# Optimization experiments

Measured on AMD Instinct MI355X. Metric: run time of the kernel, lower is better.

## Reference

```python
import jax, jax.numpy as jnp
import numpy as np

N_ATOMS = 50000
N_EDGES = 1_600_000
N_MOL = 500
HIDDEN = 128
FILTERS = 128
GAUSS = 50
LAYERS = 3
CUTOFF = 10.0
LOG2 = 0.6931471805599453


def ssp(x):
    # ShiftedSoftplus: softplus(x) - log(2)
    return jax.nn.softplus(x) - LOG2


def setup_inputs() -> dict:
    key = jax.random.key(0)
    ks = jax.random.split(key, 24)
    z = jax.random.randint(ks[0], (N_ATOMS,), 0, 100)
    pos = jax.random.uniform(ks[1], (N_ATOMS, 3), jnp.float32) * 5.0  # box keeps d < cutoff
    batch = jnp.sort(jax.random.randint(ks[2], (N_ATOMS,), 0, N_MOL))
    row = jax.random.randint(ks[3], (N_EDGES,), 0, N_ATOMS)
    off = jax.random.randint(ks[4], (N_EDGES,), 1, N_ATOMS)
    col = (row + off) % N_ATOMS  # guarantees row != col (no zero distances)
    edge_index = jnp.stack([row, col])
    def lin(k, fi, fo):
        return jax.random.normal(k, (fi, fo), jnp.float32) * (1.0 / np.sqrt(fi))
    emb = jax.random.normal(ks[5], (100, HIDDEN), jnp.float32)
    mlp1_w = jnp.stack([lin(jax.random.fold_in(ks[6], i), GAUSS, FILTERS) for i in range(LAYERS)])
    mlp1_b = jnp.zeros((LAYERS, FILTERS), jnp.float32)
    mlp2_w = jnp.stack([lin(jax.random.fold_in(ks[7], i), FILTERS, FILTERS) for i in range(LAYERS)])
    mlp2_b = jnp.zeros((LAYERS, FILTERS), jnp.float32)
    lin1_w = jnp.stack([lin(jax.random.fold_in(ks[8], i), HIDDEN, FILTERS) for i in range(LAYERS)])
    lin2_w = jnp.stack([lin(jax.random.fold_in(ks[9], i), FILTERS, HIDDEN) for i in range(LAYERS)])
    lin2_b = jnp.zeros((LAYERS, HIDDEN), jnp.float32)
    int_w = jnp.stack([lin(jax.random.fold_in(ks[10], i), HIDDEN, HIDDEN) for i in range(LAYERS)])
    int_b = jnp.zeros((LAYERS, HIDDEN), jnp.float32)
    out1_w = lin(ks[11], HIDDEN, HIDDEN // 2)
    out1_b = jnp.zeros((HIDDEN // 2,), jnp.float32)
    out2_w = lin(ks[12], HIDDEN // 2, 1)
    out2_b = jnp.zeros((1,), jnp.float32)
    return {"z": z, "pos": pos, "batch": batch, "edge_index": edge_index,
            "emb": emb, "mlp1_w": mlp1_w, "mlp1_b": mlp1_b, "mlp2_w": mlp2_w, "mlp2_b": mlp2_b,
            "lin1_w": lin1_w, "lin2_w": lin2_w, "lin2_b": lin2_b, "int_w": int_w, "int_b": int_b,
            "out1_w": out1_w, "out1_b": out1_b, "out2_w": out2_w, "out2_b": out2_b}


def reference(z, pos, batch, edge_index, emb, mlp1_w, mlp1_b, mlp2_w, mlp2_b,
              lin1_w, lin2_w, lin2_b, int_w, int_b, out1_w, out1_b, out2_w, out2_b):
    row, col = edge_index[0], edge_index[1]  # source j, target i
    d = jnp.linalg.norm(pos[row] - pos[col], axis=-1)  # [E]
    # GaussianSmearing
    offset = jnp.linspace(0.0, CUTOFF, GAUSS)
    coeff = -0.5 / (offset[1] - offset[0]) ** 2
    rbf = jnp.exp(coeff * (d[:, None] - offset[None, :]) ** 2)  # [E, GAUSS]
    # cosine cutoff
    C = 0.5 * (jnp.cos(d * jnp.pi / CUTOFF) + 1.0)  # [E]
    h = emb[z]  # [N, H]
    for l in range(LAYERS):
        W = ssp(rbf @ mlp1_w[l] + mlp1_b[l]) @ mlp2_w[l] + mlp2_b[l]  # [E, F]
        W = W * C[:, None]
        x = h @ lin1_w[l]                 # [N, F]
        msg = x[row] * W                  # gather from source, per-edge filter
        agg = jax.ops.segment_sum(msg, col, num_segments=N_ATOMS)  # scatter-add to targets
        x = agg @ lin2_w[l] + lin2_b[l]
        x = ssp(x)
        x = x @ int_w[l] + int_b[l]
        h = h + x                         # residual
    h = ssp(h @ out1_w + out1_b)
    h = h @ out2_w + out2_b               # [N, 1] per-atom energy
    out = jax.ops.segment_sum(h[:, 0], batch, num_segments=N_MOL)  # 'add' readout
    return out.reshape(-1)
```

## Files before the change

kernel.cpp:

```cpp
#include <hip/hip_runtime.h>
#include <math.h>

#define HID 128
#define NGAUSS 50
#define TBL 2048
#define TBL2 8192
#define DMAX 8.6605f
#define LDX 136
#define PGRID 768

typedef _Float16 h4 __attribute__((ext_vector_type(4)));
typedef _Float16 f16x8 __attribute__((ext_vector_type(8)));
typedef float f32x4 __attribute__((ext_vector_type(4)));

__device__ __forceinline__ float sspf(float x) {
  float ax = fabsf(x);
  return fmaxf(x, 0.0f) + log1pf(expf(-ax)) - 0.69314718055994530942f;
}

__global__ __launch_bounds__(128) void build_table_k(
    const float* __restrict__ w1, const float* __restrict__ b1,
    const float* __restrict__ w2, const float* __restrict__ b2,
    float* __restrict__ tab) {
  int l = blockIdx.x >> 11;
  int ti = blockIdx.x & (TBL - 1);
  int j = threadIdx.x;
  __shared__ float rbf[NGAUSS];
  __shared__ float v1[HID];
  const float step = DMAX / (float)(TBL - 1);
  float d = ti * step;
  if (j < NGAUSS) {
    const float gstep = 10.0f / 49.0f;
    const float gcoeff = -12.005f;
    float diff = d - j * gstep;
    rbf[j] = expf(gcoeff * diff * diff);
  }
  __syncthreads();
  float s = b1[l * HID + j];
  const float* w1p = w1 + l * NGAUSS * HID + j;
  for (int g = 0; g < NGAUSS; g++) s = fmaf(rbf[g], w1p[g * HID], s);
  v1[j] = sspf(s);
  __syncthreads();
  float s2 = b2[l * HID + j];
  const float* w2p = w2 + l * HID * HID + j;
  for (int k = 0; k < HID; k++) s2 = fmaf(v1[k], w2p[k * HID], s2);
  float C = 0.5f * (cosf(d * 0.3141592653589793f) + 1.0f);
  tab[((size_t)l * TBL + ti) * HID + j] = s2 * C;
}

__global__ __launch_bounds__(256) void upsample_k(
    const float* __restrict__ tab, _Float16* __restrict__ tabh) {
  int idx = blockIdx.x * 256 + threadIdx.x;
  if (idx >= 3 * TBL2 * HID) return;
  int ch = idx & 127;
  int i = (idx >> 7) & (TBL2 - 1);
  int l = idx >> 20;
  float t = (float)i * ((float)(TBL - 1) / (float)(TBL2 - 1));
  int i0 = min((int)t, TBL - 2);
  float f = t - (float)i0;
  const float* base = tab + ((size_t)l * TBL + i0) * HID + ch;
  tabh[idx] = (_Float16)fmaf(f, base[HID] - base[0], base[0]);
}

__global__ __launch_bounds__(256) void wswz10_k(
    const float* __restrict__ lin1, const float* __restrict__ lin2,
    const float* __restrict__ intw, const float* __restrict__ out1w,
    _Float16* __restrict__ out) {
  int b = blockIdx.x;
  int t = threadIdx.x;
  if (b < 9) {
    const float* src = (b < 3 ? lin1 : (b < 6 ? lin2 : intw)) + (size_t)(b % 3) * HID * HID;
    _Float16* dst = out + (size_t)b * 16384;
    for (int i = t; i < 16384; i += 256) {
      int j = i & 7;
      int lane = (i >> 3) & 63;
      int kk = (i >> 9) & 3;
      int ntc = i >> 11;
      int n = ntc * 16 + (lane & 15);
      int k = kk * 32 + (lane >> 4) * 8 + j;
      dst[i] = (_Float16)src[k * HID + n];
    }
  } else {
    _Float16* dst = out + (size_t)9 * 16384;
    for (int i = t; i < 8192; i += 256) {
      int j = i & 7;
      int lane = (i >> 3) & 63;
      int kk = (i >> 9) & 3;
      int ntc = i >> 11;
      int n = ntc * 16 + (lane & 15);
      int k = kk * 32 + (lane >> 4) * 8 + j;
      dst[i] = (_Float16)out1w[k * 64 + n];
    }
  }
}

__global__ __launch_bounds__(256) void emb_gather_k(
    const int* __restrict__ z, const float* __restrict__ emb,
    float* __restrict__ h, int N) {
  int i4 = blockIdx.x * 256 + threadIdx.x;
  if (i4 >= N * 32) return;
  int a = i4 >> 5;
  ((float4*)h)[i4] = ((const float4*)emb)[z[a] * 32 + (i4 & 31)];
}

__global__ __launch_bounds__(256) void bcount_k(
    const int* __restrict__ col, int* __restrict__ bcount, int E, int nbuck) {
  __shared__ int hist[1024];
  int t = threadIdx.x;
  int e0 = blockIdx.x * 2048;
  for (int j = t; j < nbuck; j += 256) hist[j] = 0;
  __syncthreads();
#pragma unroll
  for (int u = 0; u < 8; u++) {
    int e = e0 + u * 256 + t;
    if (e < E) atomicAdd(&hist[col[e] >> 6], 1);
  }
  __syncthreads();
  for (int j = t; j < nbuck; j += 256)
    if (hist[j]) atomicAdd(&bcount[j], hist[j]);
}

__global__ __launch_bounds__(256) void bucket_scan_k(
    const int* __restrict__ bcount, int* __restrict__ bstart,
    int* __restrict__ bcur, int nbuck, int* __restrict__ starts, int N) {
  __shared__ int sh[256];
  int t = threadIdx.x;
  int chunk = (nbuck + 255) / 256;
  int b0 = t * chunk;
  int c[8];
  int s = 0;
  for (int j = 0; j < chunk; j++) {
    int idx = b0 + j;
    int v = (idx < nbuck) ? bcount[idx] : 0;
    c[j] = v;
    s += v;
  }
  sh[t] = s;
  __syncthreads();
  for (int o = 1; o < 256; o <<= 1) {
    int v = (t >= o) ? sh[t - o] : 0;
    __syncthreads();
    sh[t] += v;
    __syncthreads();
  }
  int p = (t == 0) ? 0 : sh[t - 1];
  for (int j = 0; j < chunk; j++) {
    int idx = b0 + j;
    if (idx < nbuck) {
      bstart[idx] = p;
      bcur[idx] = p;
      p += c[j];
    }
  }
  if (t == 255) {
    bstart[nbuck] = p;
    starts[N] = p;
  }
}

__global__ __launch_bounds__(256) void scatterA_k(
    const int* __restrict__ row, const int* __restrict__ col,
    const float* __restrict__ pos, int* __restrict__ bcur,
    unsigned long long* __restrict__ tmp, int E, int nbuck) {
  __shared__ int hist[1024];
  __shared__ int base[1024];
  int t = threadIdx.x;
  int e0 = blockIdx.x * 2048;
  for (int j = t; j < nbuck; j += 256) hist[j] = 0;
  __syncthreads();
  int bkt[8];
  int rnk[8];
  unsigned long long key[8];
#pragma unroll
  for (int u = 0; u < 8; u++) {
    int e = e0 + u * 256 + t;
    bkt[u] = -1;
    if (e < E) {
      int r = row[e], c = col[e];
      float dx = pos[r * 3 + 0] - pos[c * 3 + 0];
      float dy = pos[r * 3 + 1] - pos[c * 3 + 1];
      float dz = pos[r * 3 + 2] - pos[c * 3 + 2];
      float d = sqrtf(dx * dx + dy * dy + dz * dz);
      const float inv2 = (float)(TBL2 - 1) / DMAX;
      int q = min((int)(d * inv2 + 0.5f), TBL2 - 1);
      unsigned int pay = ((unsigned int)r << 13) | (unsigned int)q;
      key[u] = ((unsigned long long)pay << 6) | (unsigned long long)(c & 63);
      bkt[u] = c >> 6;
      rnk[u] = atomicAdd(&hist[bkt[u]], 1);
    }
  }
  __syncthreads();
  for (int j = t; j < nbuck; j += 256)
    base[j] = hist[j] ? atomicAdd(&bcur[j], hist[j]) : 0;
  __syncthreads();
#pragma unroll
  for (int u = 0; u < 8; u++)
    if (bkt[u] >= 0) tmp[(size_t)base[bkt[u]] + rnk[u]] = key[u];
}

__global__ __launch_bounds__(256) void scatterB_k(
    const unsigned long long* __restrict__ tmp, const int* __restrict__ bstart,
    int* __restrict__ starts, unsigned int* __restrict__ payload, int N) {
  int j = blockIdx.x;
  int t = threadIdx.x;
  __shared__ int cnt[64];
  __shared__ int cur[64];
  int rs = bstart[j], re = bstart[j + 1];
  if (t < 64) cnt[t] = 0;
  __syncthreads();
  for (int e = rs + t; e < re; e += 256)
    atomicAdd(&cnt[(int)(tmp[e] & 63)], 1);
  __syncthreads();
  if (t < 64) {
    int mine = cnt[t];
    int v = mine;
    for (int o = 1; o < 64; o <<= 1) {
      int u = __shfl_up(v, o, 64);
      if (t >= o) v += u;
    }
    int excl = v - mine;
    int c = j * 64 + t;
    if (c < N) starts[c] = rs + excl;
    cur[t] = rs + excl;
  }
  __syncthreads();
  for (int e = rs + t; e < re; e += 256) {
    unsigned long long k = tmp[e];
    int p = atomicAdd(&cur[(int)(k & 63)], 1);
    payload[p] = (unsigned int)(k >> 6);
  }
}


__global__ __launch_bounds__(256) void lin1_p_k(
    const float* __restrict__ h, const _Float16* __restrict__ Wsw,
    _Float16* __restrict__ x16, int N, int ntiles) {
  __shared__ __align__(16) _Float16 Ws[16384];
  __shared__ __align__(16) _Float16 Xs[32 * LDX];
  __shared__ __align__(16) _Float16 Ys[32 * LDX];
  int t = threadIdx.x;
  int lane = t & 63, w = t >> 6;
  int g = w & 1, c = w >> 1;
  int mrow = lane & 15, quad = lane >> 4;
#pragma unroll
  for (int p = 0; p < 8; p++)
    ((uint4*)Ws)[t + p * 256] = ((const uint4*)Wsw)[t + p * 256];
  __syncthreads();
  f32x4 zero = {0.f, 0.f, 0.f, 0.f};
  for (int tile = blockIdx.x; tile < ntiles; tile += gridDim.x) {
    int a0 = tile * 32;
#pragma unroll
    for (int p = 0; p < 4; p++) {
      int id = t + p * 256;
      int a = id >> 5, kg = id & 31;
      float4 v = make_float4(0.f, 0.f, 0.f, 0.f);
      if (a0 + a < N) v = ((const float4*)h)[(size_t)(a0 + a) * 32 + kg];
      h4 o;
      o.x = (_Float16)v.x; o.y = (_Float16)v.y;
      o.z = (_Float16)v.z; o.w = (_Float16)v.w;
      *(h4*)&Xs[a * LDX + kg * 4] = o;
    }
    __syncthreads();
    f16x8 af[4];
#pragma unroll
    for (int kk = 0; kk < 4; kk++)
      af[kk] = *(const f16x8*)&Xs[(g * 16 + mrow) * LDX + kk * 32 + quad * 8];
    f32x4 acc[4];
#pragma unroll
    for (int i = 0; i < 4; i++) acc[i] = zero;
#pragma unroll
    for (int kk = 0; kk < 4; kk++) {
#pragma unroll
      for (int nt = 0; nt < 4; nt++) {
        f16x8 bf = *(const f16x8*)&Ws[(((c * 4 + nt) * 4 + kk) << 9) + lane * 8];
        acc[nt] = __builtin_amdgcn_mfma_f32_16x16x32_f16(af[kk], bf, acc[nt], 0, 0, 0);
      }
    }
#pragma unroll
    for (int nt = 0; nt < 4; nt++) {
      int colv = c * 64 + nt * 16 + mrow;
#pragma unroll
      for (int r = 0; r < 4; r++)
        Ys[(g * 16 + quad * 4 + r) * LDX + colv] = (_Float16)acc[nt][r];
    }
    __syncthreads();
#pragma unroll
    for (int p = 0; p < 2; p++) {
      int id = t + p * 256;
      int a = id >> 4, kg = id & 15;
      if (a0 + a < N)
        ((uint4*)x16)[(size_t)(a0 + a) * 16 + kg] = *(uint4*)&Ys[a * LDX + kg * 8];
    }
  }
}

__global__ __launch_bounds__(256) void ssp_p_k(
    const _Float16* __restrict__ agg16, const _Float16* __restrict__ Wsw,
    const float* __restrict__ bias, _Float16* __restrict__ y16, int N, int ntiles) {
  __shared__ __align__(16) _Float16 Ws[16384];
  __shared__ __align__(16) _Float16 Xs[32 * LDX];
  __shared__ __align__(16) _Float16 Ys[32 * LDX];
  int t = threadIdx.x;
  int lane = t & 63, w = t >> 6;
  int g = w & 1, c = w >> 1;
  int mrow = lane & 15, quad = lane >> 4;
#pragma unroll
  for (int p = 0; p < 8; p++)
    ((uint4*)Ws)[t + p * 256] = ((const uint4*)Wsw)[t + p * 256];
  float br[4];
#pragma unroll
  for (int nt = 0; nt < 4; nt++) br[nt] = bias[c * 64 + nt * 16 + mrow];
  __syncthreads();
  f32x4 zero = {0.f, 0.f, 0.f, 0.f};
  for (int tile = blockIdx.x; tile < ntiles; tile += gridDim.x) {
    int a0 = tile * 32;
#pragma unroll
    for (int p = 0; p < 2; p++) {
      int id = t + p * 256;
      int a = id >> 4, kg = id & 15;
      uint4 v = make_uint4(0, 0, 0, 0);
      if (a0 + a < N) v = ((const uint4*)agg16)[(size_t)(a0 + a) * 16 + kg];
      *(uint4*)&Xs[a * LDX + kg * 8] = v;
    }
    __syncthreads();
    f16x8 af[4];
#pragma unroll
    for (int kk = 0; kk < 4; kk++)
      af[kk] = *(const f16x8*)&Xs[(g * 16 + mrow) * LDX + kk * 32 + quad * 8];
    f32x4 acc[4];
#pragma unroll
    for (int i = 0; i < 4; i++) acc[i] = zero;
#pragma unroll
    for (int kk = 0; kk < 4; kk++) {
#pragma unroll
      for (int nt = 0; nt < 4; nt++) {
        f16x8 bf = *(const f16x8*)&Ws[(((c * 4 + nt) * 4 + kk) << 9) + lane * 8];
        acc[nt] = __builtin_amdgcn_mfma_f32_16x16x32_f16(af[kk], bf, acc[nt], 0, 0, 0);
      }
    }
#pragma unroll
    for (int nt = 0; nt < 4; nt++) {
      int colv = c * 64 + nt * 16 + mrow;
#pragma unroll
      for (int r = 0; r < 4; r++)
        Ys[(g * 16 + quad * 4 + r) * LDX + colv] = (_Float16)sspf(acc[nt][r] + br[nt]);
    }
    __syncthreads();
#pragma unroll
    for (int p = 0; p < 2; p++) {
      int id = t + p * 256;
      int a = id >> 4, kg = id & 15;
      if (a0 + a < N)
        ((uint4*)y16)[(size_t)(a0 + a) * 16 + kg] = *(uint4*)&Ys[a * LDX + kg * 8];
    }
  }
}

__global__ __launch_bounds__(256) void res_p_k(
    const _Float16* __restrict__ y16, const _Float16* __restrict__ Wsw,
    const float* __restrict__ bias, float* __restrict__ h, int N, int ntiles) {
  __shared__ __align__(16) _Float16 Ws[16384];
  __shared__ __align__(16) _Float16 Xs[32 * LDX];
  __shared__ __align__(16) _Float16 Ys[32 * LDX];
  int t = threadIdx.x;
  int lane = t & 63, w = t >> 6;
  int g = w & 1, c = w >> 1;
  int mrow = lane & 15, quad = lane >> 4;
#pragma unroll
  for (int p = 0; p < 8; p++)
    ((uint4*)Ws)[t + p * 256] = ((const uint4*)Wsw)[t + p * 256];
  float br[4];
#pragma unroll
  for (int nt = 0; nt < 4; nt++) br[nt] = bias[c * 64 + nt * 16 + mrow];
  __syncthreads();
  f32x4 zero = {0.f, 0.f, 0.f, 0.f};
  for (int tile = blockIdx.x; tile < ntiles; tile += gridDim.x) {
    int a0 = tile * 32;
#pragma unroll
    for (int p = 0; p < 2; p++) {
      int id = t + p * 256;
      int a = id >> 4, kg = id & 15;
      uint4 v = make_uint4(0, 0, 0, 0);
      if (a0 + a < N) v = ((const uint4*)y16)[(size_t)(a0 + a) * 16 + kg];
      *(uint4*)&Xs[a * LDX + kg * 8] = v;
    }
    __syncthreads();
    f16x8 af[4];
#pragma unroll
    for (int kk = 0; kk < 4; kk++)
      af[kk] = *(const f16x8*)&Xs[(g * 16 + mrow) * LDX + kk * 32 + quad * 8];
    f32x4 acc[4];
#pragma unroll
    for (int i = 0; i < 4; i++) acc[i] = zero;
#pragma unroll
    for (int kk = 0; kk < 4; kk++) {
#pragma unroll
      for (int nt = 0; nt < 4; nt++) {
        f16x8 bf = *(const f16x8*)&Ws[(((c * 4 + nt) * 4 + kk) << 9) + lane * 8];
        acc[nt] = __builtin_amdgcn_mfma_f32_16x16x32_f16(af[kk], bf, acc[nt], 0, 0, 0);
      }
    }
#pragma unroll
    for (int nt = 0; nt < 4; nt++) {
      int colv = c * 64 + nt * 16 + mrow;
#pragma unroll
      for (int r = 0; r < 4; r++)
        Ys[(g * 16 + quad * 4 + r) * LDX + colv] = (_Float16)(acc[nt][r] + br[nt]);
    }
    __syncthreads();
#pragma unroll
    for (int p = 0; p < 4; p++) {
      int id = t + p * 256;
      int a = id >> 5, kg = id & 31;
      if (a0 + a < N) {
        h4 yv = *(h4*)&Ys[a * LDX + kg * 4];
        float4 ho = ((const float4*)h)[(size_t)(a0 + a) * 32 + kg];
        ho.x += (float)yv.x; ho.y += (float)yv.y;
        ho.z += (float)yv.z; ho.w += (float)yv.w;
        ((float4*)h)[(size_t)(a0 + a) * 32 + kg] = ho;
      }
    }
  }
}

__global__ __launch_bounds__(256) void energy_p_k(
    const float* __restrict__ h, const _Float16* __restrict__ Wsw,
    const float* __restrict__ o1b, const float* __restrict__ o2w,
    const float* __restrict__ o2b, const int* __restrict__ batch,
    float* __restrict__ out, int N, int ntiles) {
  __shared__ __align__(16) _Float16 Ws[8192];
  __shared__ __align__(16) _Float16 Xs[32 * LDX];
  __shared__ float ebuf[32];
  int t = threadIdx.x;
  int lane = t & 63, w = t >> 6;
  int g = w & 1, c = w >> 1;
  int mrow = lane & 15, quad = lane >> 4;
#pragma unroll
  for (int p = 0; p < 4; p++)
    ((uint4*)Ws)[t + p * 256] = ((const uint4*)Wsw)[t + p * 256];
  float br[2], wr[2];
#pragma unroll
  for (int nt = 0; nt < 2; nt++) {
    int colv = c * 32 + nt * 16 + mrow;
    br[nt] = o1b[colv];
    wr[nt] = o2w[colv];
  }
  float o2b0 = o2b[0];
  if (t < 32) ebuf[t] = 0.f;
  __syncthreads();
  f32x4 zero = {0.f, 0.f, 0.f, 0.f};
  for (int tile = blockIdx.x; tile < ntiles; tile += gridDim.x) {
    int a0 = tile * 32;
#pragma unroll
    for (int p = 0; p < 4; p++) {
      int id = t + p * 256;
      int a = id >> 5, kg = id & 31;
      float4 v = make_float4(0.f, 0.f, 0.f, 0.f);
      if (a0 + a < N) v = ((const float4*)h)[(size_t)(a0 + a) * 32 + kg];
      h4 o;
      o.x = (_Float16)v.x; o.y = (_Float16)v.y;
      o.z = (_Float16)v.z; o.w = (_Float16)v.w;
      *(h4*)&Xs[a * LDX + kg * 4] = o;
    }
    __syncthreads();
    f16x8 af[4];
#pragma unroll
    for (int kk = 0; kk < 4; kk++)
      af[kk] = *(const f16x8*)&Xs[(g * 16 + mrow) * LDX + kk * 32 + quad * 8];
    f32x4 acc[2];
    acc[0] = zero; acc[1] = zero;
#pragma unroll
    for (int kk = 0; kk < 4; kk++) {
#pragma unroll
      for (int nt = 0; nt < 2; nt++) {
        f16x8 bf = *(const f16x8*)&Ws[(((c * 2 + nt) * 4 + kk) << 9) + lane * 8];
        acc[nt] = __builtin_amdgcn_mfma_f32_16x16x32_f16(af[kk], bf, acc[nt], 0, 0, 0);
      }
    }
    float ss[4] = {0.f, 0.f, 0.f, 0.f};
#pragma unroll
    for (int nt = 0; nt < 2; nt++)
#pragma unroll
      for (int r = 0; r < 4; r++) ss[r] += sspf(acc[nt][r] + br[nt]) * wr[nt];
#pragma unroll
    for (int r = 0; r < 4; r++) {
      ss[r] += __shfl_xor(ss[r], 1);
      ss[r] += __shfl_xor(ss[r], 2);
      ss[r] += __shfl_xor(ss[r], 4);
      ss[r] += __shfl_xor(ss[r], 8);
      if (mrow == 0) atomicAdd(&ebuf[g * 16 + quad * 4 + r], ss[r]);
    }
    __syncthreads();
    if (t < 32) {
      int a = a0 + t;
      if (a < N) atomicAdd(&out[batch[a]], ebuf[t] + o2b0);
      ebuf[t] = 0.f;
    }
  }
}

__global__ __launch_bounds__(256) void aggregate_k(
    const int* __restrict__ starts, const unsigned int* __restrict__ payload,
    const _Float16* __restrict__ x16, const _Float16* __restrict__ tabh,
    _Float16* __restrict__ agg16, int N) {
  int a = blockIdx.x * 4 + (threadIdx.x >> 6);
  if (a >= N) return;
  int lane = threadIdx.x & 63;
  int half = lane >> 5;
  int sl = lane & 31;
  int s = starts[a], e_end = starts[a + 1];
  float4 acc0 = make_float4(0.f, 0.f, 0.f, 0.f);
  float4 acc1 = make_float4(0.f, 0.f, 0.f, 0.f);
  auto do_edge = [&](unsigned int p, float4& acc) {
    int tq = (int)(p & 8191u);
    int r = (int)(p >> 13);
    h4 tw = *(const h4*)&tabh[(size_t)tq * HID + sl * 4];
    h4 xr = *(const h4*)&x16[(size_t)r * HID + sl * 4];
    acc.x = fmaf((float)xr.x, (float)tw.x, acc.x);
    acc.y = fmaf((float)xr.y, (float)tw.y, acc.y);
    acc.z = fmaf((float)xr.z, (float)tw.z, acc.z);
    acc.w = fmaf((float)xr.w, (float)tw.w, acc.w);
  };
  int i = s;
  for (; i + 8 <= e_end; i += 8) {
    unsigned int p0 = payload[i + half];
    unsigned int p1 = payload[i + 2 + half];
    unsigned int p2 = payload[i + 4 + half];
    unsigned int p3 = payload[i + 6 + half];
    do_edge(p0, acc0);
    do_edge(p1, acc1);
    do_edge(p2, acc0);
    do_edge(p3, acc1);
  }
  for (; i < e_end; i += 2) {
    int e = i + half;
    if (e < e_end) do_edge(payload[e], acc0);
  }
  acc0.x += acc1.x; acc0.y += acc1.y; acc0.z += acc1.z; acc0.w += acc1.w;
  acc0.x += __shfl_xor(acc0.x, 32);
  acc0.y += __shfl_xor(acc0.y, 32);
  acc0.z += __shfl_xor(acc0.z, 32);
  acc0.w += __shfl_xor(acc0.w, 32);
  if (half == 0) {
    h4 o;
    o.x = (_Float16)acc0.x; o.y = (_Float16)acc0.y;
    o.z = (_Float16)acc0.z; o.w = (_Float16)acc0.w;
    *(h4*)&agg16[(size_t)a * HID + sl * 4] = o;
  }
}

extern "C" void kernel_launch(void* const* d_in, const int* in_sizes, int n_in,
                              void* d_out, int out_size, void* d_ws, size_t ws_size,
                              hipStream_t stream) {
  const int* z = (const int*)d_in[0];
  const float* pos = (const float*)d_in[1];
  const int* batch = (const int*)d_in[2];
  const int* eidx = (const int*)d_in[3];
  const float* emb = (const float*)d_in[4];
  const float* mlp1_w = (const float*)d_in[5];
  const float* mlp1_b = (const float*)d_in[6];
  const float* mlp2_w = (const float*)d_in[7];
  const float* mlp2_b = (const float*)d_in[8];
  const float* lin1_w = (const float*)d_in[9];
  const float* lin2_w = (const float*)d_in[10];
  const float* lin2_b = (const float*)d_in[11];
  const float* int_w = (const float*)d_in[12];
  const float* int_b = (const float*)d_in[13];
  const float* out1_w = (const float*)d_in[14];
  const float* out1_b = (const float*)d_in[15];
  const float* out2_w = (const float*)d_in[16];
  const float* out2_b = (const float*)d_in[17];
  float* out = (float*)d_out;

  const int N = in_sizes[0];
  const int E = in_sizes[3] / 2;
  const int* row = eidx;
  const int* col = eidx + E;
  const int nbuck = (N + 63) / 64;
  const int ntiles = (N + 31) / 32;

  char* ws = (char*)d_ws;
  size_t off = 0;
  auto alloc = [&](size_t bytes) -> void* {
    void* p = ws + off;
    off = (off + bytes + 255) & ~(size_t)255;
    return p;
  };
  float* h = (float*)alloc((size_t)N * HID * 4);
  _Float16* x16 = (_Float16*)alloc((size_t)N * HID * 2);
  size_t agg_bytes = (size_t)N * HID * 2;
  size_t tmp_bytes = (size_t)E * 8 + 16;
  void* agg_union = alloc(agg_bytes > tmp_bytes ? agg_bytes : tmp_bytes);
  _Float16* agg16 = (_Float16*)agg_union;
  unsigned long long* tmp = (unsigned long long*)agg_union;
  unsigned int* payload = (unsigned int*)alloc((size_t)E * 4 + 16);
  int* starts = (int*)alloc((size_t)(N + 1) * 4);
  int* bcount = (int*)alloc((size_t)nbuck * 4);
  int* bstart = (int*)alloc((size_t)(nbuck + 1) * 4);
  int* bcur = (int*)alloc((size_t)nbuck * 4);
  float* tab = (float*)alloc((size_t)3 * TBL * HID * 4);
  _Float16* tabh = (_Float16*)alloc((size_t)3 * TBL2 * HID * 2);
  _Float16* Wsw = (_Float16*)alloc((size_t)10 * 16384 * 2);
  (void)ws_size;

  hipMemsetAsync(bcount, 0, (size_t)nbuck * 4, stream);
  hipMemsetAsync(out, 0, (size_t)out_size * 4, stream);

  build_table_k<<<3 * TBL, 128, 0, stream>>>(mlp1_w, mlp1_b, mlp2_w, mlp2_b, tab);
  upsample_k<<<(3 * TBL2 * HID + 255) / 256, 256, 0, stream>>>(tab, tabh);
  wswz10_k<<<10, 256, 0, stream>>>(lin1_w, lin2_w, int_w, out1_w, Wsw);
  emb_gather_k<<<(N * 32 + 255) / 256, 256, 0, stream>>>(z, emb, h, N);
  bcount_k<<<(E + 2047) / 2048, 256, 0, stream>>>(col, bcount, E, nbuck);
  bucket_scan_k<<<1, 256, 0, stream>>>(bcount, bstart, bcur, nbuck, starts, N);
  scatterA_k<<<(E + 2047) / 2048, 256, 0, stream>>>(row, col, pos, bcur, tmp, E, nbuck);
  scatterB_k<<<nbuck, 256, 0, stream>>>(tmp, bstart, starts, payload, N);

  int pg = PGRID < ntiles ? PGRID : ntiles;
  for (int l = 0; l < 3; l++) {
    lin1_p_k<<<pg, 256, 0, stream>>>(h, Wsw + (size_t)l * 16384, x16, N, ntiles);
    aggregate_k<<<(N + 3) / 4, 256, 0, stream>>>(starts, payload, x16,
                                                 tabh + (size_t)l * TBL2 * HID, agg16, N);
    ssp_p_k<<<pg, 256, 0, stream>>>(agg16, Wsw + (size_t)(3 + l) * 16384,
                                    lin2_b + (size_t)l * HID, x16, N, ntiles);
    res_p_k<<<pg, 256, 0, stream>>>(x16, Wsw + (size_t)(6 + l) * 16384,
                                    int_b + (size_t)l * HID, h, N, ntiles);
  }
  energy_p_k<<<pg, 256, 0, stream>>>(h, Wsw + (size_t)9 * 16384, out1_b, out2_w,
                                     out2_b, batch, out, N, ntiles);
}
```

Measured before the change: 620.7 us.

## Store residual hidden state in fp16 and coalesce per-molecule energy atomics

The residual hidden state h is now kept in fp16 instead of fp32 across all layers. This halves the bytes read and written by the embedding gather, the lin1, residual and energy kernels, and removes their per-element conversions. The energy readout now has one thread walk the 32 atoms of a tile and issue one atomicAdd per run of equal molecule ids instead of one per atom. The cost is precision: the residual sum accumulates in fp16 over three layers, which may increase error. The energy loop is also serial within each tile.

```diff
diff --git a/kernel.cpp b/kernel.cpp
--- a/kernel.cpp
+++ b/kernel.cpp
@@ -96,11 +96,15 @@
 
 __global__ __launch_bounds__(256) void emb_gather_k(
     const int* __restrict__ z, const float* __restrict__ emb,
-    float* __restrict__ h, int N) {
+    _Float16* __restrict__ h16, int N) {
   int i4 = blockIdx.x * 256 + threadIdx.x;
   if (i4 >= N * 32) return;
   int a = i4 >> 5;
-  ((float4*)h)[i4] = ((const float4*)emb)[z[a] * 32 + (i4 & 31)];
+  float4 v = ((const float4*)emb)[z[a] * 32 + (i4 & 31)];
+  h4 o;
+  o.x = (_Float16)v.x; o.y = (_Float16)v.y;
+  o.z = (_Float16)v.z; o.w = (_Float16)v.w;
+  ((h4*)h16)[i4] = o;
 }
 
 __global__ __launch_bounds__(256) void bcount_k(
@@ -232,9 +236,9 @@
 }
 
 
-__global__ __launch_bounds__(256) void lin1_p_k(
-    const float* __restrict__ h, const _Float16* __restrict__ Wsw,
-    _Float16* __restrict__ x16, int N, int ntiles) {
+__global__ __launch_bounds__(256) void lin_p_k(
+    const _Float16* __restrict__ in16, const _Float16* __restrict__ Wsw,
+    _Float16* __restrict__ out16, int N, int ntiles) {
   __shared__ __align__(16) _Float16 Ws[16384];
   __shared__ __align__(16) _Float16 Xs[32 * LDX];
   __shared__ __align__(16) _Float16 Ys[32 * LDX];
@@ -250,15 +254,12 @@
   for (int tile = blockIdx.x; tile < ntiles; tile += gridDim.x) {
     int a0 = tile * 32;
 #pragma unroll
-    for (int p = 0; p < 4; p++) {
+    for (int p = 0; p < 2; p++) {
       int id = t + p * 256;
-      int a = id >> 5, kg = id & 31;
-      float4 v = make_float4(0.f, 0.f, 0.f, 0.f);
-      if (a0 + a < N) v = ((const float4*)h)[(size_t)(a0 + a) * 32 + kg];
-      h4 o;
-      o.x = (_Float16)v.x; o.y = (_Float16)v.y;
-      o.z = (_Float16)v.z; o.w = (_Float16)v.w;
-      *(h4*)&Xs[a * LDX + kg * 4] = o;
+      int a = id >> 4, kg = id & 15;
+      uint4 v = make_uint4(0, 0, 0, 0);
+      if (a0 + a < N) v = ((const uint4*)in16)[(size_t)(a0 + a) * 16 + kg];
+      *(uint4*)&Xs[a * LDX + kg * 8] = v;
     }
     __syncthreads();
     f16x8 af[4];
@@ -289,7 +290,7 @@
       int id = t + p * 256;
       int a = id >> 4, kg = id & 15;
       if (a0 + a < N)
-        ((uint4*)x16)[(size_t)(a0 + a) * 16 + kg] = *(uint4*)&Ys[a * LDX + kg * 8];
+        ((uint4*)out16)[(size_t)(a0 + a) * 16 + kg] = *(uint4*)&Ys[a * LDX + kg * 8];
     }
   }
 }
@@ -358,7 +359,7 @@
 
 __global__ __launch_bounds__(256) void res_p_k(
     const _Float16* __restrict__ y16, const _Float16* __restrict__ Wsw,
-    const float* __restrict__ bias, float* __restrict__ h, int N, int ntiles) {
+    const float* __restrict__ bias, _Float16* __restrict__ h16, int N, int ntiles) {
   __shared__ __align__(16) _Float16 Ws[16384];
   __shared__ __align__(16) _Float16 Xs[32 * LDX];
   __shared__ __align__(16) _Float16 Ys[32 * LDX];
@@ -409,28 +410,30 @@
     }
     __syncthreads();
 #pragma unroll
-    for (int p = 0; p < 4; p++) {
+    for (int p = 0; p < 2; p++) {
       int id = t + p * 256;
-      int a = id >> 5, kg = id & 31;
+      int a = id >> 4, kg = id & 15;
       if (a0 + a < N) {
-        h4 yv = *(h4*)&Ys[a * LDX + kg * 4];
-        float4 ho = ((const float4*)h)[(size_t)(a0 + a) * 32 + kg];
-        ho.x += (float)yv.x; ho.y += (float)yv.y;
-        ho.z += (float)yv.z; ho.w += (float)yv.w;
-        ((float4*)h)[(size_t)(a0 + a) * 32 + kg] = ho;
+        f16x8 hv = *(f16x8*)&((uint4*)h16)[(size_t)(a0 + a) * 16 + kg];
+        f16x8 yv = *(f16x8*)&Ys[a * LDX + kg * 8];
+        f16x8 o;
+#pragma unroll
+        for (int j = 0; j < 8; j++) o[j] = (_Float16)((float)hv[j] + (float)yv[j]);
+        ((uint4*)h16)[(size_t)(a0 + a) * 16 + kg] = *(uint4*)&o;
       }
     }
   }
 }
 
 __global__ __launch_bounds__(256) void energy_p_k(
-    const float* __restrict__ h, const _Float16* __restrict__ Wsw,
+    const _Float16* __restrict__ h16, const _Float16* __restrict__ Wsw,
     const float* __restrict__ o1b, const float* __restrict__ o2w,
     const float* __restrict__ o2b, const int* __restrict__ batch,
     float* __restrict__ out, int N, int ntiles) {
   __shared__ __align__(16) _Float16 Ws[8192];
   __shared__ __align__(16) _Float16 Xs[32 * LDX];
   __shared__ float ebuf[32];
+  __shared__ int bat[32];
   int t = threadIdx.x;
   int lane = t & 63, w = t >> 6;
   int g = w & 1, c = w >> 1;
@@ -452,16 +455,14 @@
   for (int tile = blockIdx.x; tile < ntiles; tile += gridDim.x) {
     int a0 = tile * 32;
 #pragma unroll
-    for (int p = 0; p < 4; p++) {
+    for (int p = 0; p < 2; p++) {
       int id = t + p * 256;
-      int a = id >> 5, kg = id & 31;
-      float4 v = make_float4(0.f, 0.f, 0.f, 0.f);
-      if (a0 + a < N) v = ((const float4*)h)[(size_t)(a0 + a) * 32 + kg];
-      h4 o;
-      o.x = (_Float16)v.x; o.y = (_Float16)v.y;
-      o.z = (_Float16)v.z; o.w = (_Float16)v.w;
-      *(h4*)&Xs[a * LDX + kg * 4] = o;
-    }
+      int a = id >> 4, kg = id & 15;
+      uint4 v = make_uint4(0, 0, 0, 0);
+      if (a0 + a < N) v = ((const uint4*)h16)[(size_t)(a0 + a) * 16 + kg];
+      *(uint4*)&Xs[a * LDX + kg * 8] = v;
+    }
+    if (t < 32) bat[t] = (a0 + t < N) ? batch[a0 + t] : -1;
     __syncthreads();
     f16x8 af[4];
 #pragma unroll
@@ -491,10 +492,22 @@
       if (mrow == 0) atomicAdd(&ebuf[g * 16 + quad * 4 + r], ss[r]);
     }
     __syncthreads();
-    if (t < 32) {
-      int a = a0 + t;
-      if (a < N) atomicAdd(&out[batch[a]], ebuf[t] + o2b0);
-      ebuf[t] = 0.f;
+    if (t == 0) {
+      float acs = 0.f;
+      int pm = -1;
+      for (int i = 0; i < 32; i++) {
+        int m = bat[i];
+        float e = ebuf[i];
+        ebuf[i] = 0.f;
+        if (m < 0) break;
+        if (m != pm) {
+          if (pm >= 0) atomicAdd(&out[pm], acs);
+          acs = 0.f;
+          pm = m;
+        }
+        acs += e + o2b0;
+      }
+      if (pm >= 0) atomicAdd(&out[pm], acs);
     }
   }
 }
@@ -586,7 +599,7 @@
     off = (off + bytes + 255) & ~(size_t)255;
     return p;
   };
-  float* h = (float*)alloc((size_t)N * HID * 4);
+  _Float16* h16 = (_Float16*)alloc((size_t)N * HID * 2);
   _Float16* x16 = (_Float16*)alloc((size_t)N * HID * 2);
   size_t agg_bytes = (size_t)N * HID * 2;
   size_t tmp_bytes = (size_t)E * 8 + 16;
@@ -609,7 +622,7 @@
   build_table_k<<<3 * TBL, 128, 0, stream>>>(mlp1_w, mlp1_b, mlp2_w, mlp2_b, tab);
   upsample_k<<<(3 * TBL2 * HID + 255) / 256, 256, 0, stream>>>(tab, tabh);
   wswz10_k<<<10, 256, 0, stream>>>(lin1_w, lin2_w, int_w, out1_w, Wsw);
-  emb_gather_k<<<(N * 32 + 255) / 256, 256, 0, stream>>>(z, emb, h, N);
+  emb_gather_k<<<(N * 32 + 255) / 256, 256, 0, stream>>>(z, emb, h16, N);
   bcount_k<<<(E + 2047) / 2048, 256, 0, stream>>>(col, bcount, E, nbuck);
   bucket_scan_k<<<1, 256, 0, stream>>>(bcount, bstart, bcur, nbuck, starts, N);
   scatterA_k<<<(E + 2047) / 2048, 256, 0, stream>>>(row, col, pos, bcur, tmp, E, nbuck);
@@ -617,14 +630,14 @@
 
   int pg = PGRID < ntiles ? PGRID : ntiles;
   for (int l = 0; l < 3; l++) {
-    lin1_p_k<<<pg, 256, 0, stream>>>(h, Wsw + (size_t)l * 16384, x16, N, ntiles);
+    lin_p_k<<<pg, 256, 0, stream>>>(h16, Wsw + (size_t)l * 16384, x16, N, ntiles);
     aggregate_k<<<(N + 3) / 4, 256, 0, stream>>>(starts, payload, x16,
                                                  tabh + (size_t)l * TBL2 * HID, agg16, N);
     ssp_p_k<<<pg, 256, 0, stream>>>(agg16, Wsw + (size_t)(3 + l) * 16384,
                                     lin2_b + (size_t)l * HID, x16, N, ntiles);
     res_p_k<<<pg, 256, 0, stream>>>(x16, Wsw + (size_t)(6 + l) * 16384,
-                                    int_b + (size_t)l * HID, h, N, ntiles);
-  }
-  energy_p_k<<<pg, 256, 0, stream>>>(h, Wsw + (size_t)9 * 16384, out1_b, out2_w,
+                                    int_b + (size_t)l * HID, h16, N, ntiles);
+  }
+  energy_p_k<<<pg, 256, 0, stream>>>(h16, Wsw + (size_t)9 * 16384, out1_b, out2_w,
                                      out2_b, batch, out, N, ntiles);
 }
```

Measured after the change: 561.8 us. 9.5% less time.
